# Kernel tuning notes

Hardware: AMD Instinct MI355X
Metric: run time of the kernel (lower is better)

The kernel has to match this reference:

```python
import jax, jax.numpy as jnp
import numpy as np

T, B, H = 1024, 256, 256

def setup_inputs() -> dict:
    key = jax.random.key(0)
    k1, k2, k3, k4 = jax.random.split(key, 4)
    ins = jax.random.normal(k1, (T, B, H), dtype=jnp.float32)
    resets = jax.random.bernoulli(k2, 0.01, (T, B))
    h0 = jnp.zeros((B, H), dtype=jnp.float32)
    s = 1.0 / np.sqrt(H)
    Wi = jax.random.normal(k3, (H, 3 * H), dtype=jnp.float32) * s   # [r|z|n]
    bi = jnp.zeros((3 * H,), dtype=jnp.float32)
    Wh = jax.random.normal(k4, (H, 3 * H), dtype=jnp.float32) * s   # [r|z|n]
    bhn = jnp.zeros((H,), dtype=jnp.float32)
    return {"ins": ins, "resets": resets, "h0": h0,
            "Wi": Wi, "bi": bi, "Wh": Wh, "bhn": bhn}


def reference(ins, resets, h0, Wi, bi, Wh, bhn):
    """GRU scan with reset masking (flax GRUCell semantics).

    ins:    [T, B, H] float inputs (input dim == hidden dim by construction)
    resets: [T, B]    bool, True -> zero the carry before the cell
    returns ys: [T, B, H]
    """
    # Precompute input-side gate projections for all timesteps at once
    # (faithful: same math as per-step dense, just batched over T).
    gi_all = jnp.einsum('tbd,dh->tbh', ins, Wi) + bi  # [T, B, 3H]

    def step(h, xt):
        gi, rst = xt                                   # [B,3H], [B]
        h = jnp.where(rst[:, None], 0.0, h)            # reset masking
        gh = h @ Wh                                    # [B, 3H]
        ir, iz, inn = jnp.split(gi, 3, axis=-1)
        hr, hz, hn = jnp.split(gh, 3, axis=-1)
        r = jax.nn.sigmoid(ir + hr)
        z = jax.nn.sigmoid(iz + hz)
        n = jnp.tanh(inn + r * (hn + bhn))             # flax: hn branch has its own bias
        h_new = (1.0 - z) * n + z * h
        return h_new, h_new                            # GRUCell returns (new_h, new_h)

    _, ys = jax.lax.scan(step, h0, (gi_all, resets))
    return ys
```

## Files before the change

### kernel.cpp

```cpp
#include <hip/hip_runtime.h>
#include <hip/hip_fp16.h>

typedef unsigned int u32;
typedef _Float16 half2v __attribute__((ext_vector_type(2)));
typedef _Float16 half4v __attribute__((ext_vector_type(4)));
typedef _Float16 half8v __attribute__((ext_vector_type(8)));
typedef float f32x4 __attribute__((ext_vector_type(4)));

#define T_DIM 1024
#define B_DIM 256
#define H_DIM 256
#define G_DIM 768

__global__ void prep_kernel(const float* __restrict__ Wi,
                            const float* __restrict__ Wh,
                            _Float16* __restrict__ WiT,
                            _Float16* __restrict__ WhT) {
  int idx = blockIdx.x * 256 + threadIdx.x;
  const int total = G_DIM * H_DIM;
  const float* src = Wi;
  _Float16* dst = WiT;
  if (idx >= total) { idx -= total; src = Wh; dst = WhT; }
  int g = idx >> 8;
  int k = idx & 255;
  dst[idx] = (_Float16)src[(size_t)k * G_DIM + g];
}

#define BM 128
#define BN 128
#define BK 64
#define LDK 72

__global__ __launch_bounds__(256, 2) void gemm_gi_kernel(
    const float* __restrict__ A,
    const _Float16* __restrict__ BT,
    const float* __restrict__ bias,
    _Float16* __restrict__ C)
{
  __shared__ _Float16 As[BM * LDK];
  __shared__ _Float16 Bs[BN * LDK];

  const int tid  = threadIdx.x;
  const int lane = tid & 63;
  const int lc   = lane & 15;
  const int lg   = lane >> 4;
  const int wid  = tid >> 6;
  const int wr   = wid >> 1;
  const int wc   = wid & 1;

  const int id   = blockIdx.x;
  const int xcd  = id & 7;
  const int slot = id >> 3;
  const int nt   = slot % 6;
  const int mt   = (slot / 6) * 8 + xcd;
  const int m0 = mt * BM;
  const int n0 = nt * BN;

  f32x4 acc[4][4] = {};

  for (int kt = 0; kt < H_DIM; kt += BK) {
#pragma unroll
    for (int i = 0; i < 8; ++i) {
      int c   = tid + i * 256;
      int row = c >> 4;
      int kc  = (c & 15) << 2;
      const float4 v = *(const float4*)(A + (size_t)(m0 + row) * H_DIM + kt + kc);
      half4v h;
      h.x = (_Float16)v.x; h.y = (_Float16)v.y;
      h.z = (_Float16)v.z; h.w = (_Float16)v.w;
      *(half4v*)(&As[row * LDK + kc]) = h;
    }
#pragma unroll
    for (int i = 0; i < 8; ++i) {
      int c   = tid + i * 256;
      int row = c >> 4;
      int kc  = (c & 15) << 2;
      half4v v = *(const half4v*)(BT + (size_t)(n0 + row) * H_DIM + kt + kc);
      int rowp = (row & 3) * 32 + (row >> 2);
      *(half4v*)(&Bs[rowp * LDK + kc]) = v;
    }
    __syncthreads();

#pragma unroll
    for (int kk = 0; kk < 2; ++kk) {
      half8v af[4], bf[4];
#pragma unroll
      for (int m = 0; m < 4; ++m)
        af[m] = *(const half8v*)(&As[(wr*64 + m*16 + lc) * LDK + kk*32 + lg*8]);
#pragma unroll
      for (int n = 0; n < 4; ++n)
        bf[n] = *(const half8v*)(&Bs[(n*32 + wc*16 + lc) * LDK + kk*32 + lg*8]);
#pragma unroll
      for (int m = 0; m < 4; ++m)
#pragma unroll
        for (int n = 0; n < 4; ++n)
          acc[m][n] = __builtin_amdgcn_mfma_f32_16x16x32_f16(af[m], bf[n], acc[m][n], 0, 0, 0);
    }
    __syncthreads();
  }

  const int cbase = n0 + wc*64 + 4*lc;
  const float4 bv4 = *(const float4*)(bias + cbase);
#pragma unroll
  for (int m = 0; m < 4; ++m) {
#pragma unroll
    for (int q = 0; q < 4; ++q) {
      const int row = m0 + wr*64 + m*16 + lg*4 + q;
      half4v o;
      o[0] = (_Float16)(acc[m][0][q] + bv4.x);
      o[1] = (_Float16)(acc[m][1][q] + bv4.y);
      o[2] = (_Float16)(acc[m][2][q] + bv4.z);
      o[3] = (_Float16)(acc[m][3][q] + bv4.w);
      *(half4v*)(&C[(size_t)row * G_DIM + cbase]) = o;
    }
  }
}

__device__ __forceinline__ float sigmoidf_fast(float x) {
  return __builtin_amdgcn_rcpf(1.f + __expf(-x));
}
__device__ __forceinline__ float tanhf_fast(float x) {
  return 1.f - 2.f * __builtin_amdgcn_rcpf(__expf(2.f * x) + 1.f);
}

#define DOT12(HV, c)                                                  \
  asm("v_dot2_f32_f16 %0, %3, %15, %0\n\t"                            \
      "v_dot2_f32_f16 %1, %7, %15, %1\n\t"                            \
      "v_dot2_f32_f16 %2, %11, %15, %2\n\t"                           \
      "v_dot2_f32_f16 %0, %4, %16, %0\n\t"                            \
      "v_dot2_f32_f16 %1, %8, %16, %1\n\t"                            \
      "v_dot2_f32_f16 %2, %12, %16, %2\n\t"                           \
      "v_dot2_f32_f16 %0, %5, %17, %0\n\t"                            \
      "v_dot2_f32_f16 %1, %9, %17, %1\n\t"                            \
      "v_dot2_f32_f16 %2, %13, %17, %2\n\t"                           \
      "v_dot2_f32_f16 %0, %6, %18, %0\n\t"                            \
      "v_dot2_f32_f16 %1, %10, %18, %1\n\t"                           \
      "v_dot2_f32_f16 %2, %14, %18, %2"                               \
      : "+v"(aR), "+v"(aZ), "+v"(aN)                                  \
      : "v"(wR[4*(c)]), "v"(wR[4*(c)+1]), "v"(wR[4*(c)+2]), "v"(wR[4*(c)+3]), \
        "v"(wZ[4*(c)]), "v"(wZ[4*(c)+1]), "v"(wZ[4*(c)+2]), "v"(wZ[4*(c)+3]), \
        "v"(wN[4*(c)]), "v"(wN[4*(c)+1]), "v"(wN[4*(c)+2]), "v"(wN[4*(c)+3]), \
        "v"((HV).x), "v"((HV).y), "v"((HV).z), "v"((HV).w))

#define SB() __builtin_amdgcn_sched_barrier(0)

#define QSTRIDE 144

__global__ __launch_bounds__(1024, 4) void gru_scan_kernel(
    const _Float16* __restrict__ WhT,
    const _Float16* __restrict__ gi,
    const int* __restrict__ resets,
    const float* __restrict__ h0,
    const float* __restrict__ bhn,
    float* __restrict__ ys)
{
  const int b  = blockIdx.x;
  const int s  = threadIdx.x;
  const int j  = s >> 2;
  const int qt = s & 3;

  __shared__ __align__(16) char hbuf[2][4 * QSTRIDE];

  u32 wR[32], wZ[32], wN[32];
  {
    const uint4* pR = (const uint4*)(WhT + (size_t)j         * H_DIM + qt * 64);
    const uint4* pZ = (const uint4*)(WhT + (size_t)(j + 256) * H_DIM + qt * 64);
    const uint4* pN = (const uint4*)(WhT + (size_t)(j + 512) * H_DIM + qt * 64);
#pragma unroll
    for (int i = 0; i < 8; ++i) {
      uint4 v = pR[i]; wR[4*i]=v.x; wR[4*i+1]=v.y; wR[4*i+2]=v.z; wR[4*i+3]=v.w;
    }
#pragma unroll
    for (int i = 0; i < 8; ++i) {
      uint4 v = pZ[i]; wZ[4*i]=v.x; wZ[4*i+1]=v.y; wZ[4*i+2]=v.z; wZ[4*i+3]=v.w;
    }
#pragma unroll
    for (int i = 0; i < 8; ++i) {
      uint4 v = pN[i]; wN[4*i]=v.x; wN[4*i+1]=v.y; wN[4*i+2]=v.z; wN[4*i+3]=v.w;
    }
  }

  const float bn = bhn[j];

  const int region = j >> 6;
  const int carry_writer = (qt == region);
  const int ys_writer    = (qt == ((region + 1) & 3));
  const int waddr = region * QSTRIDE + (j & 63) * 2;

  float hprev;
  {
    const int r0 = resets[b];
    hprev = r0 ? 0.f : h0[(size_t)b * H_DIM + j];
    if (carry_writer) *(_Float16*)(&hbuf[0][waddr]) = (_Float16)hprev;
  }
  __syncthreads();

  const _Float16* gbase = gi + (size_t)b * G_DIM + j;
  float* yp = ys + (size_t)b * H_DIM + j;

  float gcR = (float)gbase[0];
  float gcZ = (float)gbase[256];
  float gcN = (float)gbase[512];

  int p = 0;
  for (int t = 0; t < T_DIM; ++t) {
    float aR = 0.f, aZ = 0.f, aN = 0.f;
    const char* hb = &hbuf[p][qt * QSTRIDE];

    uint4 hA = *(const uint4*)(hb);
    uint4 hB = *(const uint4*)(hb + 16);
    DOT12(hA, 0);
    SB();
    hA = *(const uint4*)(hb + 32);
    DOT12(hB, 1);
    SB();
    hB = *(const uint4*)(hb + 48);
    DOT12(hA, 2);
    SB();
    hA = *(const uint4*)(hb + 64);
    DOT12(hB, 3);
    SB();
    hB = *(const uint4*)(hb + 80);
    DOT12(hA, 4);
    SB();
    hA = *(const uint4*)(hb + 96);
    DOT12(hB, 5);
    SB();
    hB = *(const uint4*)(hb + 112);
    DOT12(hA, 6);
    DOT12(hB, 7);

    const int tn = (t + 1 < T_DIM) ? (t + 1) : (T_DIM - 1);
    const _Float16* gp = gbase + (size_t)tn * (B_DIM * G_DIM);
    const float gnR = (float)gp[0];
    const float gnZ = (float)gp[256];
    const float gnN = (float)gp[512];
    const int rstn = (t + 1 < T_DIM) ? resets[tn * B_DIM + b] : 0;

    aR += __shfl_xor(aR, 1);  aR += __shfl_xor(aR, 2);
    aZ += __shfl_xor(aZ, 1);  aZ += __shfl_xor(aZ, 2);
    aN += __shfl_xor(aN, 1);  aN += __shfl_xor(aN, 2);

    const float r  = sigmoidf_fast(aR + gcR);
    const float zg = sigmoidf_fast(aZ + gcZ);
    const float n  = tanhf_fast(gcN + r * (aN + bn));
    const float hn = (1.f - zg) * n + zg * hprev;

    const float hx = rstn ? 0.f : hn;
    if (carry_writer) {
      *(_Float16*)(&hbuf[p ^ 1][waddr]) = (_Float16)hx;
    } else if (ys_writer) {
      yp[(size_t)t * (B_DIM * H_DIM)] = hn;
    }
    hprev = hx;
    gcR = gnR; gcZ = gnZ; gcN = gnN;

    asm volatile("s_waitcnt lgkmcnt(0)\n\ts_barrier" ::: "memory");
    p ^= 1;
  }
}

__global__ void sentinel_kernel(float* out, int n) {
  int i = blockIdx.x * 256 + threadIdx.x;
  if (i < n) out[i] = 12345.0f;
}

extern "C" void kernel_launch(void* const* d_in, const int* in_sizes, int n_in,
                              void* d_out, int out_size, void* d_ws, size_t ws_size,
                              hipStream_t stream) {
  const float* ins    = (const float*)d_in[0];
  const int*   resets = (const int*)d_in[1];
  const float* h0     = (const float*)d_in[2];
  const float* Wi     = (const float*)d_in[3];
  const float* bi     = (const float*)d_in[4];
  const float* Wh     = (const float*)d_in[5];
  const float* bhn    = (const float*)d_in[6];
  float* ys = (float*)d_out;

  const size_t wbytes  = (size_t)G_DIM * H_DIM * 2;
  const size_t gibytes = (size_t)T_DIM * B_DIM * G_DIM * 2;
  const size_t need = 2 * wbytes + gibytes;
  if (ws_size < need) {
    sentinel_kernel<<<(out_size + 255) / 256, 256, 0, stream>>>(ys, out_size);
    return;
  }

  char* ws = (char*)d_ws;
  _Float16* WiT = (_Float16*)ws;
  _Float16* WhT = (_Float16*)(ws + wbytes);
  _Float16* gi  = (_Float16*)(ws + 2 * wbytes);

  prep_kernel<<<(2 * G_DIM * H_DIM) / 256, 256, 0, stream>>>(Wi, Wh, WiT, WhT);

  const int M = T_DIM * B_DIM;
  const int nblocks = (M / BM) * (G_DIM / BN);
  gemm_gi_kernel<<<nblocks, 256, 0, stream>>>(ins, WiT, bi, gi);

  gru_scan_kernel<<<B_DIM, 1024, 0, stream>>>(WhT, gi, resets, h0, bhn, ys);
}
```

Baseline: 1.843 ms.

## Keep recurrent weights in AGPRs and read them per dot chunk

Result: slower. 3.299 ms (+79.0%).

```diff
diff --git a/kernel.cpp b/kernel.cpp
--- a/kernel.cpp
+++ b/kernel.cpp
@@ -123,26 +123,43 @@
   return 1.f - 2.f * __builtin_amdgcn_rcpf(__expf(2.f * x) + 1.f);
 }
 
-#define DOT12(HV, c)                                                  \
-  asm("v_dot2_f32_f16 %0, %3, %15, %0\n\t"                            \
-      "v_dot2_f32_f16 %1, %7, %15, %1\n\t"                            \
-      "v_dot2_f32_f16 %2, %11, %15, %2\n\t"                           \
-      "v_dot2_f32_f16 %0, %4, %16, %0\n\t"                            \
-      "v_dot2_f32_f16 %1, %8, %16, %1\n\t"                            \
-      "v_dot2_f32_f16 %2, %12, %16, %2\n\t"                           \
-      "v_dot2_f32_f16 %0, %5, %17, %0\n\t"                            \
-      "v_dot2_f32_f16 %1, %9, %17, %1\n\t"                            \
-      "v_dot2_f32_f16 %2, %13, %17, %2\n\t"                           \
-      "v_dot2_f32_f16 %0, %6, %18, %0\n\t"                            \
-      "v_dot2_f32_f16 %1, %10, %18, %1\n\t"                           \
-      "v_dot2_f32_f16 %2, %14, %18, %2"                               \
-      : "+v"(aR), "+v"(aZ), "+v"(aN)                                  \
-      : "v"(wR[4*(c)]), "v"(wR[4*(c)+1]), "v"(wR[4*(c)+2]), "v"(wR[4*(c)+3]), \
-        "v"(wZ[4*(c)]), "v"(wZ[4*(c)+1]), "v"(wZ[4*(c)+2]), "v"(wZ[4*(c)+3]), \
-        "v"(wN[4*(c)]), "v"(wN[4*(c)+1]), "v"(wN[4*(c)+2]), "v"(wN[4*(c)+3]), \
-        "v"((HV).x), "v"((HV).y), "v"((HV).z), "v"((HV).w))
-
-#define SB() __builtin_amdgcn_sched_barrier(0)
+#define DOT12A(HV, c)                                                        \
+  { u32 t0, t1, t2;                                                          \
+  asm("v_accvgpr_read_b32 %3, %6\n\t"                                        \
+      "v_accvgpr_read_b32 %4, %10\n\t"                                       \
+      "v_accvgpr_read_b32 %5, %14\n\t"                                       \
+      "v_dot2_f32_f16 %0, %3, %18, %0\n\t"                                   \
+      "v_accvgpr_read_b32 %3, %7\n\t"                                        \
+      "v_dot2_f32_f16 %1, %4, %18, %1\n\t"                                   \
+      "v_accvgpr_read_b32 %4, %11\n\t"                                       \
+      "v_dot2_f32_f16 %2, %5, %18, %2\n\t"                                   \
+      "v_accvgpr_read_b32 %5, %15\n\t"                                       \
+      "v_dot2_f32_f16 %0, %3, %19, %0\n\t"                                   \
+      "v_accvgpr_read_b32 %3, %8\n\t"                                        \
+      "v_dot2_f32_f16 %1, %4, %19, %1\n\t"                                   \
+      "v_accvgpr_read_b32 %4, %12\n\t"                                       \
+      "v_dot2_f32_f16 %2, %5, %19, %2\n\t"                                   \
+      "v_accvgpr_read_b32 %5, %16\n\t"                                       \
+      "v_dot2_f32_f16 %0, %3, %20, %0\n\t"                                   \
+      "v_accvgpr_read_b32 %3, %9\n\t"                                        \
+      "v_dot2_f32_f16 %1, %4, %20, %1\n\t"                                   \
+      "v_accvgpr_read_b32 %4, %13\n\t"                                       \
+      "v_dot2_f32_f16 %2, %5, %20, %2\n\t"                                   \
+      "v_accvgpr_read_b32 %5, %17\n\t"                                       \
+      "v_dot2_f32_f16 %0, %3, %21, %0\n\t"                                   \
+      "v_dot2_f32_f16 %1, %4, %21, %1\n\t"                                   \
+      "v_dot2_f32_f16 %2, %5, %21, %2"                                       \
+      : "+v"(aR), "+v"(aZ), "+v"(aN), "=&v"(t0), "=&v"(t1), "=&v"(t2)        \
+      : "a"(wRa[4*(c)]), "a"(wRa[4*(c)+1]), "a"(wRa[4*(c)+2]), "a"(wRa[4*(c)+3]), \
+        "a"(wZa[4*(c)]), "a"(wZa[4*(c)+1]), "a"(wZa[4*(c)+2]), "a"(wZa[4*(c)+3]), \
+        "a"(wNa[4*(c)]), "a"(wNa[4*(c)+1]), "a"(wNa[4*(c)+2]), "a"(wNa[4*(c)+3]), \
+        "v"((HV).x), "v"((HV).y), "v"((HV).z), "v"((HV).w)); }
+
+#define LAUNDER4(dst, i, v)                                                  \
+  asm("v_accvgpr_write_b32 %0, %1" : "=a"(dst[4*(i)  ]) : "v"((v).x));       \
+  asm("v_accvgpr_write_b32 %0, %1" : "=a"(dst[4*(i)+1]) : "v"((v).y));       \
+  asm("v_accvgpr_write_b32 %0, %1" : "=a"(dst[4*(i)+2]) : "v"((v).z));       \
+  asm("v_accvgpr_write_b32 %0, %1" : "=a"(dst[4*(i)+3]) : "v"((v).w));
 
 #define QSTRIDE 144
 
@@ -161,23 +178,17 @@
 
   __shared__ __align__(16) char hbuf[2][4 * QSTRIDE];
 
-  u32 wR[32], wZ[32], wN[32];
+  u32 wRa[32], wZa[32], wNa[32];
   {
     const uint4* pR = (const uint4*)(WhT + (size_t)j         * H_DIM + qt * 64);
     const uint4* pZ = (const uint4*)(WhT + (size_t)(j + 256) * H_DIM + qt * 64);
     const uint4* pN = (const uint4*)(WhT + (size_t)(j + 512) * H_DIM + qt * 64);
 #pragma unroll
-    for (int i = 0; i < 8; ++i) {
-      uint4 v = pR[i]; wR[4*i]=v.x; wR[4*i+1]=v.y; wR[4*i+2]=v.z; wR[4*i+3]=v.w;
-    }
-#pragma unroll
-    for (int i = 0; i < 8; ++i) {
-      uint4 v = pZ[i]; wZ[4*i]=v.x; wZ[4*i+1]=v.y; wZ[4*i+2]=v.z; wZ[4*i+3]=v.w;
-    }
-#pragma unroll
-    for (int i = 0; i < 8; ++i) {
-      uint4 v = pN[i]; wN[4*i]=v.x; wN[4*i+1]=v.y; wN[4*i+2]=v.z; wN[4*i+3]=v.w;
-    }
+    for (int i = 0; i < 8; ++i) { uint4 v = pR[i]; LAUNDER4(wRa, i, v); }
+#pragma unroll
+    for (int i = 0; i < 8; ++i) { uint4 v = pZ[i]; LAUNDER4(wZa, i, v); }
+#pragma unroll
+    for (int i = 0; i < 8; ++i) { uint4 v = pN[i]; LAUNDER4(wNa, i, v); }
   }
 
   const float bn = bhn[j];
@@ -204,38 +215,32 @@
 
   int p = 0;
   for (int t = 0; t < T_DIM; ++t) {
-    float aR = 0.f, aZ = 0.f, aN = 0.f;
-    const char* hb = &hbuf[p][qt * QSTRIDE];
-
-    uint4 hA = *(const uint4*)(hb);
-    uint4 hB = *(const uint4*)(hb + 16);
-    DOT12(hA, 0);
-    SB();
-    hA = *(const uint4*)(hb + 32);
-    DOT12(hB, 1);
-    SB();
-    hB = *(const uint4*)(hb + 48);
-    DOT12(hA, 2);
-    SB();
-    hA = *(const uint4*)(hb + 64);
-    DOT12(hB, 3);
-    SB();
-    hB = *(const uint4*)(hb + 80);
-    DOT12(hA, 4);
-    SB();
-    hA = *(const uint4*)(hb + 96);
-    DOT12(hB, 5);
-    SB();
-    hB = *(const uint4*)(hb + 112);
-    DOT12(hA, 6);
-    DOT12(hB, 7);
-
     const int tn = (t + 1 < T_DIM) ? (t + 1) : (T_DIM - 1);
     const _Float16* gp = gbase + (size_t)tn * (B_DIM * G_DIM);
     const float gnR = (float)gp[0];
     const float gnZ = (float)gp[256];
     const float gnN = (float)gp[512];
     const int rstn = (t + 1 < T_DIM) ? resets[tn * B_DIM + b] : 0;
+
+    float aR = 0.f, aZ = 0.f, aN = 0.f;
+    const char* hb = &hbuf[p][qt * QSTRIDE];
+
+    uint4 hA = *(const uint4*)(hb);
+    uint4 hB = *(const uint4*)(hb + 16);
+    DOT12A(hA, 0);
+    hA = *(const uint4*)(hb + 32);
+    DOT12A(hB, 1);
+    hB = *(const uint4*)(hb + 48);
+    DOT12A(hA, 2);
+    hA = *(const uint4*)(hb + 64);
+    DOT12A(hB, 3);
+    hB = *(const uint4*)(hb + 80);
+    DOT12A(hA, 4);
+    hA = *(const uint4*)(hb + 96);
+    DOT12A(hB, 5);
+    hB = *(const uint4*)(hb + 112);
+    DOT12A(hA, 6);
+    DOT12A(hB, 7);
 
     aR += __shfl_xor(aR, 1);  aR += __shfl_xor(aR, 2);
     aZ += __shfl_xor(aZ, 1);  aZ += __shfl_xor(aZ, 2);
```
